# Kernel tuning notes

Measured on AMD Instinct MI355X. Metric: run time of the kernel, lower is better.

The kernel has to match this reference:

```python
import jax, jax.numpy as jnp
import numpy as np
import math

C = 512
HEADS = 8
GROUPS = 32
HIDDEN = C * 4
EPS = 1e-5


def group_norm(x, gamma, beta, groups, eps=EPS):
    # x: (b, c, *spatial). Normalize per (sample, group) over (c//g, *spatial).
    b, c = x.shape[0], x.shape[1]
    xg = x.reshape(b, groups, -1)
    mean = xg.mean(axis=-1, keepdims=True)
    var = xg.var(axis=-1, keepdims=True)
    xg = (xg - mean) * jax.lax.rsqrt(var + eps)
    xn = xg.reshape(x.shape)
    shape = (1, c) + (1,) * (x.ndim - 2)
    return xn * gamma.reshape(shape) + beta.reshape(shape)


def setup_inputs() -> dict:
    key = jax.random.key(0)
    ks = jax.random.split(key, 10)
    s = lambda fan_in: 1.0 / math.sqrt(fan_in)
    inp = {
        "x": jax.random.normal(ks[0], (8, C, 32, 32), dtype=jnp.float32),
        "gn1_gamma": jnp.ones((C,), jnp.float32),
        "gn1_beta": jnp.zeros((C,), jnp.float32),
        "qkv_w": jax.random.uniform(ks[1], (3 * C, C), jnp.float32, -s(C), s(C)),
        "qkv_b": jax.random.uniform(ks[2], (3 * C,), jnp.float32, -s(C), s(C)),
        "out_w": jax.random.uniform(ks[3], (C, C), jnp.float32, -s(C), s(C)),
        "out_b": jax.random.uniform(ks[4], (C,), jnp.float32, -s(C), s(C)),
        "gn2_gamma": jnp.ones((C,), jnp.float32),
        "gn2_beta": jnp.zeros((C,), jnp.float32),
        "mlp1_w": jax.random.uniform(ks[5], (2 * HIDDEN, C), jnp.float32, -s(C), s(C)),
        "mlp2_w": jax.random.uniform(ks[6], (C, HIDDEN), jnp.float32, -s(HIDDEN), s(HIDDEN)),
    }
    return inp


def reference(x, gn1_gamma, gn1_beta, qkv_w, qkv_b, out_w, out_b,
              gn2_gamma, gn2_beta, mlp1_w, mlp2_w):
    b, c, h, w = x.shape
    n = h * w
    head_dim = c // HEADS
    x_norm = group_norm(x, gn1_gamma, gn1_beta, GROUPS).reshape(b, c, n)
    # 1x1 conv1d == channel matmul
    qkv = jnp.einsum('oc,bcn->bon', qkv_w, x_norm) + qkv_b[None, :, None]
    q, k, v = jnp.split(qkv, 3, axis=1)
    split_heads = lambda t: t.reshape(b, HEADS, head_dim, n).transpose(0, 1, 3, 2)  # b h n d
    q, k, v = split_heads(q), split_heads(k), split_heads(v)
    attn = jnp.einsum('bhnd,bhmd->bhnm', q, k) / math.sqrt(head_dim)
    attn = jax.nn.softmax(attn, axis=-1)  # internally max-stabilized
    x_attn = jnp.einsum('bhnm,bhmd->bhnd', attn, v)
    x_attn = x_attn.transpose(0, 1, 3, 2).reshape(b, c, n)  # b (h d) n
    x_attn = jnp.einsum('oc,bcn->bon', out_w, x_attn) + out_b[None, :, None]
    x_attn = group_norm(x_attn, gn2_gamma, gn2_beta, GROUPS)
    x_attn = x_attn.transpose(0, 2, 1)  # b n c
    hgate = x_attn @ mlp1_w.T  # b n 2*hidden
    h1, gate = jnp.split(hgate, 2, axis=-1)
    x_attn = jax.nn.silu(h1) * gate
    x_attn = x_attn @ mlp2_w.T  # b n c
    x_attn = x_attn.transpose(0, 2, 1).reshape(b, c, h, w)
    return x + x_attn
```

## Files before the change

### kernel.cpp

```cpp
#include <hip/hip_runtime.h>

typedef unsigned short ushort_t;
typedef __bf16 bf16x8 __attribute__((ext_vector_type(8)));
typedef float f32x4 __attribute__((ext_vector_type(4)));
typedef unsigned short u16x8 __attribute__((ext_vector_type(8)));
typedef unsigned short u16x4 __attribute__((ext_vector_type(4)));
typedef unsigned int __attribute__((address_space(1))) as1_uint;
typedef unsigned int __attribute__((address_space(3))) as3_uint;

#define DEV __device__ __forceinline__

DEV float bf2f(ushort_t u) { union { float f; unsigned i; } c; c.i = (unsigned)u << 16; return c.f; }
DEV ushort_t f2bf(float f) {
  union { float f; unsigned i; } c; c.f = f;
  return (ushort_t)((c.i + 0x7FFFu + ((c.i >> 16) & 1u)) >> 16);
}

DEV f32x4 mfma16(bf16x8 a, bf16x8 b, f32x4 c) {
  return __builtin_amdgcn_mfma_f32_16x16x32_bf16(a, b, c, 0, 0, 0);
}

DEV void g2lds16(const void* g, void* l) {
  __builtin_amdgcn_global_load_lds((as1_uint*)g, (as3_uint*)l, 16, 0, 0);
}

DEV void xcd_swz(int gx, int gy, int& bx, int& by) {
  int nwg = gx * gy;
  int wg = by * gx + bx;
  int q = nwg >> 3, r = nwg & 7;
  int xcd = wg & 7, idx = wg >> 3;
  int swz = (xcd < r ? xcd * (q + 1) : r * (q + 1) + (xcd - r) * q) + idx;
  bx = swz % gx;
  by = swz / gx;
}

__global__ __launch_bounds__(256) void cvt_all(const float* __restrict__ w0, const float* __restrict__ w1,
                                               const float* __restrict__ w2, const float* __restrict__ w3,
                                               ushort_t* __restrict__ o0, ushort_t* __restrict__ o1,
                                               ushort_t* __restrict__ o2, ushort_t* __restrict__ o3) {
  int i = blockIdx.x * 256 + threadIdx.x;
  const float* src; ushort_t* dst; int base;
  if (i < 196608)      { src = w0; dst = o0; base = 0; }
  else if (i < 262144) { src = w1; dst = o1; base = 196608; }
  else if (i < 786432) { src = w2; dst = o2; base = 262144; }
  else                 { src = w3; dst = o3; base = 786432; }
  int j = i - base;
  float4 v = ((const float4*)src)[j];
  u16x4 o;
  o[0] = f2bf(v.x); o[1] = f2bf(v.y); o[2] = f2bf(v.z); o[3] = f2bf(v.w);
  ((u16x4*)dst)[j] = o;
}

__global__ __launch_bounds__(256) void gn_stats_cn(const float* __restrict__ x, float* __restrict__ st) {
  int b = blockIdx.x >> 5, g = blockIdx.x & 31;
  const float4* base = (const float4*)(x + ((size_t)b * 512 + g * 16) * 1024);
  float s = 0.f, sq = 0.f;
  for (int i = threadIdx.x; i < 4096; i += 256) {
    float4 v = base[i];
    s += v.x + v.y + v.z + v.w;
    sq += v.x * v.x + v.y * v.y + v.z * v.z + v.w * v.w;
  }
  #pragma unroll
  for (int mk = 1; mk < 64; mk <<= 1) { s += __shfl_xor(s, mk); sq += __shfl_xor(sq, mk); }
  __shared__ float red[8];
  if ((threadIdx.x & 63) == 0) { red[(threadIdx.x >> 6) * 2] = s; red[(threadIdx.x >> 6) * 2 + 1] = sq; }
  __syncthreads();
  if (threadIdx.x == 0) {
    s = red[0] + red[2] + red[4] + red[6];
    sq = red[1] + red[3] + red[5] + red[7];
    float mean = s * (1.f / 16384.f);
    float var = sq * (1.f / 16384.f) - mean * mean;
    st[blockIdx.x * 2] = mean;
    st[blockIdx.x * 2 + 1] = rsqrtf(var + 1e-5f);
  }
}

__global__ __launch_bounds__(256) void gn_stats_nc(const ushort_t* __restrict__ OP, float* __restrict__ st) {
  int b = blockIdx.x >> 5, g = blockIdx.x & 31;
  float s = 0.f, sq = 0.f;
  for (int jj = threadIdx.x; jj < 2048; jj += 256) {
    int n = jj >> 1, c8 = (jj & 1) * 8;
    u16x8 v = *(const u16x8*)(OP + (size_t)(b * 1024 + n) * 512 + g * 16 + c8);
    #pragma unroll
    for (int t = 0; t < 8; ++t) { float f = bf2f(v[t]); s += f; sq += f * f; }
  }
  #pragma unroll
  for (int mk = 1; mk < 64; mk <<= 1) { s += __shfl_xor(s, mk); sq += __shfl_xor(sq, mk); }
  __shared__ float red[8];
  if ((threadIdx.x & 63) == 0) { red[(threadIdx.x >> 6) * 2] = s; red[(threadIdx.x >> 6) * 2 + 1] = sq; }
  __syncthreads();
  if (threadIdx.x == 0) {
    s = red[0] + red[2] + red[4] + red[6];
    sq = red[1] + red[3] + red[5] + red[7];
    float mean = s * (1.f / 16384.f);
    float var = sq * (1.f / 16384.f) - mean * mean;
    st[blockIdx.x * 2] = mean;
    st[blockIdx.x * 2 + 1] = rsqrtf(var + 1e-5f);
  }
}

__global__ __launch_bounds__(256) void gn1_norm_t(const float* __restrict__ x, const float* __restrict__ st,
                                                  const float* __restrict__ gamma, const float* __restrict__ beta,
                                                  ushort_t* __restrict__ XN) {
  __shared__ float tile[64][65];
  int b = blockIdx.z, c0 = blockIdx.y * 64, n0 = blockIdx.x * 64;
  int tx = threadIdx.x & 63, ty = threadIdx.x >> 6;
  for (int i = ty; i < 64; i += 4) {
    int c = c0 + i;
    float mean = st[(b * 32 + (c >> 4)) * 2], rstd = st[(b * 32 + (c >> 4)) * 2 + 1];
    float v = x[((size_t)b * 512 + c) * 1024 + n0 + tx];
    tile[i][tx] = (v - mean) * rstd * gamma[c] + beta[c];
  }
  __syncthreads();
  for (int j = ty; j < 64; j += 4)
    XN[(size_t)(b * 1024 + n0 + j) * 512 + c0 + tx] = f2bf(tile[tx][j]);
}

__global__ __launch_bounds__(256) void transpose_v(const ushort_t* __restrict__ QKVT, ushort_t* __restrict__ VT) {
  __shared__ ushort_t tile[64][65];
  int b = blockIdx.z, c0 = blockIdx.y * 64, n0 = blockIdx.x * 64;
  int tx = threadIdx.x & 63, ty = threadIdx.x >> 6;
  for (int j = ty; j < 64; j += 4)
    tile[j][tx] = QKVT[(size_t)(b * 1024 + n0 + j) * 1536 + 1024 + c0 + tx];
  __syncthreads();
  for (int i = ty; i < 64; i += 4)
    VT[((size_t)b * 512 + c0 + i) * 1024 + n0 + tx] = tile[tx][i];
}

__global__ __launch_bounds__(256) void gn2_norm(const ushort_t* __restrict__ OP, const float* __restrict__ st,
                                                const float* __restrict__ gamma, const float* __restrict__ beta,
                                                ushort_t* __restrict__ XN2) {
  size_t idx = ((size_t)blockIdx.x * 256 + threadIdx.x) * 8;
  int c0 = (int)(idx & 511);
  int gi = (int)(idx >> 9);
  int b = gi >> 10;
  int g = c0 >> 4;
  float mean = st[(b * 32 + g) * 2], rstd = st[(b * 32 + g) * 2 + 1];
  u16x8 v = *(const u16x8*)(OP + idx);
  u16x8 o;
  #pragma unroll
  for (int t = 0; t < 8; ++t) {
    int c = c0 + t;
    o[t] = f2bf((bf2f(v[t]) - mean) * rstd * gamma[c] + beta[c]);
  }
  *(u16x8*)(XN2 + idx) = o;
}

template <int EPI, bool DBUF>
__global__ __launch_bounds__(256) void gemm_bt(const ushort_t* __restrict__ A, int lda,
                                               const ushort_t* __restrict__ B, int ldb,
                                               const float* __restrict__ bias,
                                               void* __restrict__ Out, int ldo, int K,
                                               const float* __restrict__ resid) {
  constexpr int NJ = 2;
  constexpr int BN = NJ * 32;
  constexpr int NB = DBUF ? 2 : 1;
  __shared__ __align__(16) ushort_t As[NB][128 * 64];
  __shared__ __align__(16) ushort_t Bs[NB][BN * 64];
  const int tid = threadIdx.x;
  const int lane = tid & 63, wave = tid >> 6;
  const int l15 = lane & 15, l4 = lane >> 4;
  int bx = blockIdx.x, by = blockIdx.y;
  xcd_swz(gridDim.x, gridDim.y, bx, by);
  const int m0 = by * 128, n0 = bx * BN;
  const int wr = (wave >> 1) * 64, wc = (wave & 1) * (NJ * 16);
  f32x4 acc[4][NJ] = {};

  auto stage = [&](int bufi, int kk) {
    #pragma unroll
    for (int p = 0; p < 4; ++p) {
      int s = p * 256 + wave * 64 + lane;
      int row = s >> 3, c8 = (s & 7) * 8;
      g2lds16(A + (size_t)(m0 + row) * lda + kk + c8, (char*)As[bufi] + (p * 256 + wave * 64) * 16);
    }
    #pragma unroll
    for (int p = 0; p < NJ; ++p) {
      int s = p * 256 + wave * 64 + lane;
      int row = s >> 3, c8 = (s & 7) * 8;
      g2lds16(B + (size_t)(n0 + row) * ldb + kk + c8, (char*)Bs[bufi] + (p * 256 + wave * 64) * 16);
    }
  };
  auto compute = [&](int bufi) {
    const ushort_t* Asb = As[bufi];
    const ushort_t* Bsb = Bs[bufi];
    #pragma unroll
    for (int ks = 0; ks < 2; ++ks) {
      bf16x8 af[4], bfr[NJ];
      #pragma unroll
      for (int i = 0; i < 4; ++i)
        af[i] = *(const bf16x8*)(Asb + (wr + i * 16 + l15) * 64 + ks * 32 + l4 * 8);
      #pragma unroll
      for (int j = 0; j < NJ; ++j)
        bfr[j] = *(const bf16x8*)(Bsb + (wc + j * 16 + l15) * 64 + ks * 32 + l4 * 8);
      #pragma unroll
      for (int i = 0; i < 4; ++i)
        #pragma unroll
        for (int j = 0; j < NJ; ++j)
          acc[i][j] = mfma16(af[i], bfr[j], acc[i][j]);
    }
  };

  if constexpr (DBUF) {
    stage(0, 0);
    __syncthreads();
    int cur = 0;
    for (int k0 = 0; k0 < K; k0 += 64) {
      if (k0 + 64 < K) stage(cur ^ 1, k0 + 64);
      compute(cur);
      __syncthreads();
      cur ^= 1;
    }
  } else {
    for (int k0 = 0; k0 < K; k0 += 64) {
      stage(0, k0);
      __syncthreads();
      compute(0);
      __syncthreads();
    }
  }

  #pragma unroll
  for (int i = 0; i < 4; ++i) {
    #pragma unroll
    for (int j = 0; j < NJ; ++j) {
      int row = m0 + wr + i * 16 + l4 * 4;
      int col = n0 + wc + j * 16 + l15;
      if constexpr (EPI == 0) {
        float bv = bias ? bias[col] : 0.f;
        ushort_t* o = (ushort_t*)Out;
        #pragma unroll
        for (int r = 0; r < 4; ++r)
          o[(size_t)(row + r) * ldo + col] = f2bf(acc[i][j][r] + bv);
      } else {
        int bb = row >> 10, n = row & 1023;
        size_t idx = ((size_t)bb * 512 + col) * 1024 + n;
        float4 rv = *(const float4*)(resid + idx);
        float4 ov = make_float4(acc[i][j][0] + rv.x, acc[i][j][1] + rv.y,
                                acc[i][j][2] + rv.z, acc[i][j][3] + rv.w);
        *(float4*)((float*)Out + idx) = ov;
      }
    }
  }
}

__global__ __launch_bounds__(256) void gemm_mlp1(const ushort_t* __restrict__ A,
                                                 const ushort_t* __restrict__ B1,
                                                 const ushort_t* __restrict__ B2,
                                                 ushort_t* __restrict__ Out) {
  __shared__ __align__(16) ushort_t As[128 * 64];
  __shared__ __align__(16) ushort_t B1s[64 * 64];
  __shared__ __align__(16) ushort_t B2s[64 * 64];
  const int tid = threadIdx.x;
  const int lane = tid & 63, wave = tid >> 6;
  const int l15 = lane & 15, l4 = lane >> 4;
  int bx = blockIdx.x, by = blockIdx.y;
  xcd_swz(gridDim.x, gridDim.y, bx, by);
  const int m0 = by * 128, n0 = bx * 64;
  const int wr = (wave >> 1) * 64, wc = (wave & 1) * 32;
  f32x4 acc1[4][2] = {};
  f32x4 acc2[4][2] = {};
  for (int k0 = 0; k0 < 512; k0 += 64) {
    #pragma unroll
    for (int p = 0; p < 4; ++p) {
      int s = p * 256 + wave * 64 + lane;
      int row = s >> 3, c8 = (s & 7) * 8;
      g2lds16(A + (size_t)(m0 + row) * 512 + k0 + c8, (char*)As + (p * 256 + wave * 64) * 16);
    }
    #pragma unroll
    for (int p = 0; p < 2; ++p) {
      int s = p * 256 + wave * 64 + lane;
      int row = s >> 3, c8 = (s & 7) * 8;
      g2lds16(B1 + (size_t)(n0 + row) * 512 + k0 + c8, (char*)B1s + (p * 256 + wave * 64) * 16);
      g2lds16(B2 + (size_t)(n0 + row) * 512 + k0 + c8, (char*)B2s + (p * 256 + wave * 64) * 16);
    }
    __syncthreads();
    #pragma unroll
    for (int ks = 0; ks < 2; ++ks) {
      bf16x8 af[4], b1f[2], b2f[2];
      #pragma unroll
      for (int i = 0; i < 4; ++i)
        af[i] = *(const bf16x8*)(As + (wr + i * 16 + l15) * 64 + ks * 32 + l4 * 8);
      #pragma unroll
      for (int j = 0; j < 2; ++j) {
        b1f[j] = *(const bf16x8*)(B1s + (wc + j * 16 + l15) * 64 + ks * 32 + l4 * 8);
        b2f[j] = *(const bf16x8*)(B2s + (wc + j * 16 + l15) * 64 + ks * 32 + l4 * 8);
      }
      #pragma unroll
      for (int i = 0; i < 4; ++i)
        #pragma unroll
        for (int j = 0; j < 2; ++j) {
          acc1[i][j] = mfma16(af[i], b1f[j], acc1[i][j]);
          acc2[i][j] = mfma16(af[i], b2f[j], acc2[i][j]);
        }
    }
    __syncthreads();
  }
  #pragma unroll
  for (int i = 0; i < 4; ++i) {
    #pragma unroll
    for (int j = 0; j < 2; ++j) {
      int row = m0 + wr + i * 16 + l4 * 4;
      int col = n0 + wc + j * 16 + l15;
      #pragma unroll
      for (int r = 0; r < 4; ++r) {
        float h1 = acc1[i][j][r];
        float sg = h1 / (1.f + __expf(-h1));
        Out[(size_t)(row + r) * 2048 + col] = f2bf(sg * acc2[i][j][r]);
      }
    }
  }
}

__global__ __launch_bounds__(512, 4) void attn_kernel(const ushort_t* __restrict__ QKVT,
                                                      const ushort_t* __restrict__ VT,
                                                      ushort_t* __restrict__ AT) {
  __shared__ __align__(16) ushort_t Kt[2][64 * 64];
  __shared__ __align__(16) ushort_t Vt[2][64 * 64];
  __shared__ __align__(16) ushort_t Pl[8][16 * 64];
  const int tid = threadIdx.x, lane = tid & 63, wave = tid >> 6;
  const int l15 = lane & 15, l4 = lane >> 4;
  int bx = blockIdx.x, by = blockIdx.y;
  xcd_swz(gridDim.x, gridDim.y, bx, by);
  const int b = bx >> 3, h = bx & 7;
  const int qr0 = by * 128 + wave * 16;
  bf16x8 qf[2];
  #pragma unroll
  for (int ks = 0; ks < 2; ++ks)
    qf[ks] = *(const bf16x8*)(QKVT + (size_t)(b * 1024 + qr0 + l15) * 1536 + h * 64 + ks * 32 + l4 * 8);
  f32x4 acc_o[4] = {};
  float mst[4], lst[4];
  #pragma unroll
  for (int r = 0; r < 4; ++r) { mst[r] = -1e30f; lst[r] = 0.f; }
  const float scale = 0.125f;

  auto stage = [&](int bufi, int m0) {
    int s = tid;
    int row = s >> 3, c8 = ((s & 7) ^ (row & 7)) * 8;
    g2lds16(QKVT + (size_t)(b * 1024 + m0 + row) * 1536 + 512 + h * 64 + c8,
            (char*)Kt[bufi] + (wave * 64) * 16);
    g2lds16(VT + ((size_t)b * 512 + h * 64 + row) * 1024 + m0 + c8,
            (char*)Vt[bufi] + (wave * 64) * 16);
  };

  stage(0, 0);
  __syncthreads();
  int cur = 0;
  for (int t = 0; t < 16; ++t) {
    if (t < 15) stage(cur ^ 1, (t + 1) * 64);
    const ushort_t* Ktb = Kt[cur];
    const ushort_t* Vtb = Vt[cur];
    f32x4 accs[4] = {};
    __builtin_amdgcn_s_setprio(1);
    #pragma unroll
    for (int ks = 0; ks < 2; ++ks) {
      #pragma unroll
      for (int j = 0; j < 4; ++j) {
        bf16x8 kf = *(const bf16x8*)(Ktb + (j * 16 + l15) * 64 + (((ks * 4 + l4) ^ (l15 & 7)) << 3));
        accs[j] = mfma16(qf[ks], kf, accs[j]);
      }
    }
    __builtin_amdgcn_s_setprio(0);
    float tm[4], al[4], rs[4];
    #pragma unroll
    for (int r = 0; r < 4; ++r) {
      float t0 = fmaxf(fmaxf(accs[0][r], accs[1][r]), fmaxf(accs[2][r], accs[3][r]));
      tm[r] = t0 * scale;
    }
    #pragma unroll
    for (int mk = 1; mk < 16; mk <<= 1)
      #pragma unroll
      for (int r = 0; r < 4; ++r)
        tm[r] = fmaxf(tm[r], __shfl_xor(tm[r], mk));
    #pragma unroll
    for (int r = 0; r < 4; ++r) {
      float mn = fmaxf(mst[r], tm[r]);
      al[r] = __expf(mst[r] - mn);
      mst[r] = mn;
      rs[r] = 0.f;
    }
    #pragma unroll
    for (int j = 0; j < 4; ++j)
      #pragma unroll
      for (int r = 0; r < 4; ++r) {
        float pv = __expf(accs[j][r] * scale - mst[r]);
        accs[j][r] = pv;
        rs[r] += pv;
      }
    #pragma unroll
    for (int mk = 1; mk < 16; mk <<= 1)
      #pragma unroll
      for (int r = 0; r < 4; ++r)
        rs[r] += __shfl_xor(rs[r], mk);
    #pragma unroll
    for (int r = 0; r < 4; ++r) lst[r] = lst[r] * al[r] + rs[r];
    #pragma unroll
    for (int jd = 0; jd < 4; ++jd)
      #pragma unroll
      for (int r = 0; r < 4; ++r) acc_o[jd][r] *= al[r];
    #pragma unroll
    for (int j = 0; j < 4; ++j)
      #pragma unroll
      for (int r = 0; r < 4; ++r) {
        int prow = l4 * 4 + r, pcol = j * 16 + l15;
        Pl[wave][prow * 64 + ((((pcol >> 3) ^ (prow & 7)) << 3) | (pcol & 7))] = f2bf(accs[j][r]);
      }
    __builtin_amdgcn_s_setprio(1);
    #pragma unroll
    for (int km = 0; km < 2; ++km) {
      bf16x8 pf = *(const bf16x8*)(&Pl[wave][l15 * 64 + (((km * 4 + l4) ^ (l15 & 7)) << 3)]);
      #pragma unroll
      for (int jd = 0; jd < 4; ++jd) {
        bf16x8 vf = *(const bf16x8*)(Vtb + (jd * 16 + l15) * 64 + (((km * 4 + l4) ^ (l15 & 7)) << 3));
        acc_o[jd] = mfma16(pf, vf, acc_o[jd]);
      }
    }
    __builtin_amdgcn_s_setprio(0);
    __syncthreads();
    cur ^= 1;
  }
  float inv[4];
  #pragma unroll
  for (int r = 0; r < 4; ++r) inv[r] = 1.f / lst[r];
  #pragma unroll
  for (int jd = 0; jd < 4; ++jd)
    #pragma unroll
    for (int r = 0; r < 4; ++r)
      AT[(size_t)(b * 1024 + qr0 + l4 * 4 + r) * 512 + h * 64 + jd * 16 + l15] =
          f2bf(acc_o[jd][r] * inv[r]);
}

extern "C" void kernel_launch(void* const* d_in, const int* in_sizes, int n_in,
                              void* d_out, int out_size, void* d_ws, size_t ws_size,
                              hipStream_t stream) {
  const float* x    = (const float*)d_in[0];
  const float* g1   = (const float*)d_in[1];
  const float* b1   = (const float*)d_in[2];
  const float* qkvw = (const float*)d_in[3];
  const float* qkvb = (const float*)d_in[4];
  const float* outw = (const float*)d_in[5];
  const float* outb = (const float*)d_in[6];
  const float* g2   = (const float*)d_in[7];
  const float* b2   = (const float*)d_in[8];
  const float* m1w  = (const float*)d_in[9];
  const float* m2w  = (const float*)d_in[10];

  char* ws = (char*)d_ws;
  const size_t MB = 1ull << 20;
  ushort_t* XN   = (ushort_t*)(ws + 0);
  ushort_t* QKVT = (ushort_t*)(ws + 8 * MB);
  ushort_t* VT   = (ushort_t*)(ws + 32 * MB);
  ushort_t* AT   = (ushort_t*)(ws + 40 * MB);
  ushort_t* OP   = (ushort_t*)(ws + 48 * MB);
  ushort_t* XN2  = (ushort_t*)(ws + 0);
  ushort_t* HID  = (ushort_t*)(ws + 8 * MB);
  ushort_t* WQ   = (ushort_t*)(ws + 88 * MB);
  ushort_t* WO   = (ushort_t*)(ws + 90 * MB);
  ushort_t* WM1  = (ushort_t*)(ws + 91 * MB);
  ushort_t* WM2  = (ushort_t*)(ws + 96 * MB);
  float*    ST1  = (float*)(ws + 99 * MB);
  float*    ST2  = (float*)(ws + 99 * MB + 4096);

  cvt_all<<<4096, 256, 0, stream>>>(qkvw, outw, m1w, m2w, WQ, WO, WM1, WM2);

  gn_stats_cn<<<256, 256, 0, stream>>>(x, ST1);
  gn1_norm_t<<<dim3(16, 8, 8), 256, 0, stream>>>(x, ST1, g1, b1, XN);

  gemm_bt<0, false><<<dim3(24, 64), 256, 0, stream>>>(XN, 512, WQ, 512, qkvb, QKVT, 1536, 512, nullptr);
  transpose_v<<<dim3(16, 8, 8), 256, 0, stream>>>(QKVT, VT);
  attn_kernel<<<dim3(64, 8), 512, 0, stream>>>(QKVT, VT, AT);

  gemm_bt<0, true><<<dim3(8, 64), 256, 0, stream>>>(AT, 512, WO, 512, outb, OP, 512, 512, nullptr);
  gn_stats_nc<<<256, 256, 0, stream>>>(OP, ST2);
  gn2_norm<<<2048, 256, 0, stream>>>(OP, ST2, g2, b2, XN2);

  gemm_mlp1<<<dim3(32, 64), 256, 0, stream>>>(XN2, WM1, WM1 + 2048 * 512, HID);

  gemm_bt<1, true><<<dim3(8, 64), 256, 0, stream>>>(HID, 2048, WM2, 2048, nullptr, d_out, 0, 2048, x);
}
```

Baseline: 327.9 us.

## Double-buffer QKV and MLP1 GEMMs, drop XCD block swizzle

The QKV projection GEMM and the fused MLP1 GEMM now use two LDS buffers, so the next K tile loads while the current one is computed. This replaces the old stage-sync-compute-sync loop and is meant to hide global-load latency. The XCD-aware block remapping is also removed from every GEMM and the attention kernel, which trades L2 locality across chiplets for a simpler index computation. gemm_mlp1's LDS use doubles to 64KB, which may lower occupancy.

After: 315.7 us. 3.7% less time.

```diff
diff --git a/kernel.cpp b/kernel.cpp
--- a/kernel.cpp
+++ b/kernel.cpp
@@ -22,16 +22,6 @@
 
 DEV void g2lds16(const void* g, void* l) {
   __builtin_amdgcn_global_load_lds((as1_uint*)g, (as3_uint*)l, 16, 0, 0);
-}
-
-DEV void xcd_swz(int gx, int gy, int& bx, int& by) {
-  int nwg = gx * gy;
-  int wg = by * gx + bx;
-  int q = nwg >> 3, r = nwg & 7;
-  int xcd = wg & 7, idx = wg >> 3;
-  int swz = (xcd < r ? xcd * (q + 1) : r * (q + 1) + (xcd - r) * q) + idx;
-  bx = swz % gx;
-  by = swz / gx;
 }
 
 __global__ __launch_bounds__(256) void cvt_all(const float* __restrict__ w0, const float* __restrict__ w1,
@@ -146,7 +136,7 @@
   *(u16x8*)(XN2 + idx) = o;
 }
 
-template <int EPI, bool DBUF>
+template <int EPI>
 __global__ __launch_bounds__(256) void gemm_bt(const ushort_t* __restrict__ A, int lda,
                                                const ushort_t* __restrict__ B, int ldb,
                                                const float* __restrict__ bias,
@@ -154,15 +144,12 @@
                                                const float* __restrict__ resid) {
   constexpr int NJ = 2;
   constexpr int BN = NJ * 32;
-  constexpr int NB = DBUF ? 2 : 1;
-  __shared__ __align__(16) ushort_t As[NB][128 * 64];
-  __shared__ __align__(16) ushort_t Bs[NB][BN * 64];
+  __shared__ __align__(16) ushort_t As[2][128 * 64];
+  __shared__ __align__(16) ushort_t Bs[2][BN * 64];
   const int tid = threadIdx.x;
   const int lane = tid & 63, wave = tid >> 6;
   const int l15 = lane & 15, l4 = lane >> 4;
-  int bx = blockIdx.x, by = blockIdx.y;
-  xcd_swz(gridDim.x, gridDim.y, bx, by);
-  const int m0 = by * 128, n0 = bx * BN;
+  const int m0 = blockIdx.y * 128, n0 = blockIdx.x * BN;
   const int wr = (wave >> 1) * 64, wc = (wave & 1) * (NJ * 16);
   f32x4 acc[4][NJ] = {};
 
@@ -200,23 +187,14 @@
     }
   };
 
-  if constexpr (DBUF) {
-    stage(0, 0);
+  stage(0, 0);
+  __syncthreads();
+  int cur = 0;
+  for (int k0 = 0; k0 < K; k0 += 64) {
+    if (k0 + 64 < K) stage(cur ^ 1, k0 + 64);
+    compute(cur);
     __syncthreads();
-    int cur = 0;
-    for (int k0 = 0; k0 < K; k0 += 64) {
-      if (k0 + 64 < K) stage(cur ^ 1, k0 + 64);
-      compute(cur);
-      __syncthreads();
-      cur ^= 1;
-    }
-  } else {
-    for (int k0 = 0; k0 < K; k0 += 64) {
-      stage(0, k0);
-      __syncthreads();
-      compute(0);
-      __syncthreads();
-    }
+    cur ^= 1;
   }
 
   #pragma unroll
@@ -247,43 +225,46 @@
                                                  const ushort_t* __restrict__ B1,
                                                  const ushort_t* __restrict__ B2,
                                                  ushort_t* __restrict__ Out) {
-  __shared__ __align__(16) ushort_t As[128 * 64];
-  __shared__ __align__(16) ushort_t B1s[64 * 64];
-  __shared__ __align__(16) ushort_t B2s[64 * 64];
+  __shared__ __align__(16) ushort_t As[2][128 * 64];
+  __shared__ __align__(16) ushort_t B1s[2][64 * 64];
+  __shared__ __align__(16) ushort_t B2s[2][64 * 64];
   const int tid = threadIdx.x;
   const int lane = tid & 63, wave = tid >> 6;
   const int l15 = lane & 15, l4 = lane >> 4;
-  int bx = blockIdx.x, by = blockIdx.y;
-  xcd_swz(gridDim.x, gridDim.y, bx, by);
-  const int m0 = by * 128, n0 = bx * 64;
+  const int m0 = blockIdx.y * 128, n0 = blockIdx.x * 64;
   const int wr = (wave >> 1) * 64, wc = (wave & 1) * 32;
   f32x4 acc1[4][2] = {};
   f32x4 acc2[4][2] = {};
-  for (int k0 = 0; k0 < 512; k0 += 64) {
+
+  auto stage = [&](int bufi, int kk) {
     #pragma unroll
     for (int p = 0; p < 4; ++p) {
       int s = p * 256 + wave * 64 + lane;
       int row = s >> 3, c8 = (s & 7) * 8;
-      g2lds16(A + (size_t)(m0 + row) * 512 + k0 + c8, (char*)As + (p * 256 + wave * 64) * 16);
+      g2lds16(A + (size_t)(m0 + row) * 512 + kk + c8, (char*)As[bufi] + (p * 256 + wave * 64) * 16);
     }
     #pragma unroll
     for (int p = 0; p < 2; ++p) {
       int s = p * 256 + wave * 64 + lane;
       int row = s >> 3, c8 = (s & 7) * 8;
-      g2lds16(B1 + (size_t)(n0 + row) * 512 + k0 + c8, (char*)B1s + (p * 256 + wave * 64) * 16);
-      g2lds16(B2 + (size_t)(n0 + row) * 512 + k0 + c8, (char*)B2s + (p * 256 + wave * 64) * 16);
-    }
-    __syncthreads();
+      g2lds16(B1 + (size_t)(n0 + row) * 512 + kk + c8, (char*)B1s[bufi] + (p * 256 + wave * 64) * 16);
+      g2lds16(B2 + (size_t)(n0 + row) * 512 + kk + c8, (char*)B2s[bufi] + (p * 256 + wave * 64) * 16);
+    }
+  };
+  auto compute = [&](int bufi) {
+    const ushort_t* Asb = As[bufi];
+    const ushort_t* B1b = B1s[bufi];
+    const ushort_t* B2b = B2s[bufi];
     #pragma unroll
     for (int ks = 0; ks < 2; ++ks) {
       bf16x8 af[4], b1f[2], b2f[2];
       #pragma unroll
       for (int i = 0; i < 4; ++i)
-        af[i] = *(const bf16x8*)(As + (wr + i * 16 + l15) * 64 + ks * 32 + l4 * 8);
+        af[i] = *(const bf16x8*)(Asb + (wr + i * 16 + l15) * 64 + ks * 32 + l4 * 8);
       #pragma unroll
       for (int j = 0; j < 2; ++j) {
-        b1f[j] = *(const bf16x8*)(B1s + (wc + j * 16 + l15) * 64 + ks * 32 + l4 * 8);
-        b2f[j] = *(const bf16x8*)(B2s + (wc + j * 16 + l15) * 64 + ks * 32 + l4 * 8);
+        b1f[j] = *(const bf16x8*)(B1b + (wc + j * 16 + l15) * 64 + ks * 32 + l4 * 8);
+        b2f[j] = *(const bf16x8*)(B2b + (wc + j * 16 + l15) * 64 + ks * 32 + l4 * 8);
       }
       #pragma unroll
       for (int i = 0; i < 4; ++i)
@@ -293,8 +274,18 @@
           acc2[i][j] = mfma16(af[i], b2f[j], acc2[i][j]);
         }
     }
+  };
+
+  stage(0, 0);
+  __syncthreads();
+  int cur = 0;
+  for (int k0 = 0; k0 < 512; k0 += 64) {
+    if (k0 + 64 < 512) stage(cur ^ 1, k0 + 64);
+    compute(cur);
     __syncthreads();
-  }
+    cur ^= 1;
+  }
+
   #pragma unroll
   for (int i = 0; i < 4; ++i) {
     #pragma unroll
@@ -319,10 +310,8 @@
   __shared__ __align__(16) ushort_t Pl[8][16 * 64];
   const int tid = threadIdx.x, lane = tid & 63, wave = tid >> 6;
   const int l15 = lane & 15, l4 = lane >> 4;
-  int bx = blockIdx.x, by = blockIdx.y;
-  xcd_swz(gridDim.x, gridDim.y, bx, by);
-  const int b = bx >> 3, h = bx & 7;
-  const int qr0 = by * 128 + wave * 16;
+  const int b = blockIdx.x >> 3, h = blockIdx.x & 7;
+  const int qr0 = blockIdx.y * 128 + wave * 16;
   bf16x8 qf[2];
   #pragma unroll
   for (int ks = 0; ks < 2; ++ks)
@@ -465,15 +454,15 @@
   gn_stats_cn<<<256, 256, 0, stream>>>(x, ST1);
   gn1_norm_t<<<dim3(16, 8, 8), 256, 0, stream>>>(x, ST1, g1, b1, XN);
 
-  gemm_bt<0, false><<<dim3(24, 64), 256, 0, stream>>>(XN, 512, WQ, 512, qkvb, QKVT, 1536, 512, nullptr);
+  gemm_bt<0><<<dim3(24, 64), 256, 0, stream>>>(XN, 512, WQ, 512, qkvb, QKVT, 1536, 512, nullptr);
   transpose_v<<<dim3(16, 8, 8), 256, 0, stream>>>(QKVT, VT);
   attn_kernel<<<dim3(64, 8), 512, 0, stream>>>(QKVT, VT, AT);
 
-  gemm_bt<0, true><<<dim3(8, 64), 256, 0, stream>>>(AT, 512, WO, 512, outb, OP, 512, 512, nullptr);
+  gemm_bt<0><<<dim3(8, 64), 256, 0, stream>>>(AT, 512, WO, 512, outb, OP, 512, 512, nullptr);
   gn_stats_nc<<<256, 256, 0, stream>>>(OP, ST2);
   gn2_norm<<<2048, 256, 0, stream>>>(OP, ST2, g2, b2, XN2);
 
   gemm_mlp1<<<dim3(32, 64), 256, 0, stream>>>(XN2, WM1, WM1 + 2048 * 512, HID);
 
-  gemm_bt<1, true><<<dim3(8, 64), 256, 0, stream>>>(HID, 2048, WM2, 2048, nullptr, d_out, 0, 2048, x);
-}
+  gemm_bt<1><<<dim3(8, 64), 256, 0, stream>>>(HID, 2048, WM2, 2048, nullptr, d_out, 0, 2048, x);
+}
```
